# Optimization experiments

Hardware: AMD Instinct MI355X
Metric: run time of the kernel (lower is better)

The kernel has to match this reference:

```python
import jax, jax.numpy as jnp
import numpy as np

B, T, D = 256, 128, 300
H = 512          # lstm_size
NUM_LAYERS = 2
OUT_DIM = 200    # context_encoded_dim
FORGET_BIAS = 1.0


def lstm_layer(x, W, b):
    """BasicLSTMCell over time. x: [B,T,in], W: [in+H,4H], b: [4H] -> [B,T,H].
    Gate order i, j, f, o (TF BasicLSTMCell); c' = c*sig(f+1) + sig(i)*tanh(j)."""
    Bn = x.shape[0]
    c0 = jnp.zeros((Bn, H), x.dtype)
    h0 = jnp.zeros((Bn, H), x.dtype)

    def step(carry, xt):
        c, h = carry
        z = jnp.concatenate([xt, h], axis=-1) @ W + b  # [B,4H]
        i, j, f, o = jnp.split(z, 4, axis=-1)
        c = c * jax.nn.sigmoid(f + FORGET_BIAS) + jax.nn.sigmoid(i) * jnp.tanh(j)
        h = jnp.tanh(c) * jax.nn.sigmoid(o)
        return (c, h), h

    _, hs = jax.lax.scan(step, (c0, h0), jnp.swapaxes(x, 0, 1))  # [T,B,H]
    return jnp.swapaxes(hs, 0, 1)  # [B,T,H]


def encode(x, W0, b0, W1, b1, lengths):
    h = lstm_layer(x, W0, b0)
    h = lstm_layer(h, W1, b1)
    # last valid output per example (dynamic_rnn outputs before `length` are
    # identical to a plain scan; we gather at t = length-1)
    idx = (lengths - 1).astype(jnp.int32)[:, None, None]  # [B,1,1]
    return jnp.take_along_axis(h, idx, axis=1)[:, 0, :]   # [B,H]


def setup_inputs() -> dict:
    key = jax.random.key(0)
    ks = jax.random.split(key, 12)
    s = 1.0 / 100.0

    def gate_w(k, in_dim):
        return jax.random.normal(k, (in_dim + H, 4 * H), jnp.float32) * 0.05

    return {
        "left_embed": jax.random.normal(ks[0], (B, T, D), jnp.float32),
        "right_embed": jax.random.normal(ks[1], (B, T, D), jnp.float32),
        "left_lengths": jax.random.randint(ks[2], (B,), 1, T + 1, jnp.int32),
        "right_lengths": jax.random.randint(ks[3], (B,), 1, T + 1, jnp.int32),
        "lW0": gate_w(ks[4], D),
        "lb0": jnp.zeros((4 * H,), jnp.float32),
        "lW1": gate_w(ks[5], H),
        "lb1": jnp.zeros((4 * H,), jnp.float32),
        "rW0": gate_w(ks[6], D),
        "rb0": jnp.zeros((4 * H,), jnp.float32),
        "rW1": gate_w(ks[7], H),
        "rb1": jnp.zeros((4 * H,), jnp.float32),
        "trans_W": jax.random.normal(ks[8], (2 * H, OUT_DIM), jnp.float32) * s,
    }


def reference(left_embed, right_embed, left_lengths, right_lengths,
              lW0, lb0, lW1, lb1, rW0, rb0, rW1, rb1, trans_W):
    left_last = encode(left_embed, lW0, lb0, lW1, lb1, left_lengths)    # [B,H]
    right_last = encode(right_embed, rW0, rb0, rW1, rb1, right_lengths)  # [B,H]
    ctx = jnp.concatenate([left_last, right_last], axis=1)  # [B,2H]
    return ctx @ trans_W  # [B,OUT_DIM]; dropout keep_prob=1.0 -> identity
```

## Files before the change

### kernel.cpp

```cpp
#include <hip/hip_runtime.h>
#include <hip/hip_bf16.h>
#include <stdint.h>


using short4_t = __attribute__((ext_vector_type(4))) short;
using short8_t = __attribute__((ext_vector_type(8))) short;
using f32x4    = __attribute__((ext_vector_type(4))) float;
using ull2_t   = __attribute__((ext_vector_type(2))) unsigned long long;

#define B_   256
#define T_   128
#define Draw 300
#define Dp   320
#define H_   512
#define G4   2048
#define TC   8
#define MC   (TC * 256)
#define NC   (T_ / TC)
#define FLAG_STRIDE 64

__device__ __forceinline__ short f2bf(float x){
  union { float f; unsigned u; } v; v.f = x;
  unsigned r = (v.u + 0x7FFFu + ((v.u >> 16) & 1u)) >> 16;
  return (short)r;
}
__device__ __forceinline__ float bf2f(short b){
  union { unsigned u; float f; } v; v.u = ((unsigned)(unsigned short)b) << 16;
  return v.f;
}
__device__ __forceinline__ float sigf(float x){ return 1.f / (1.f + __expf(-x)); }
__device__ __forceinline__ float tanh_f(float x){
  x = fmaxf(-15.f, fminf(15.f, x));
  float e = __expf(-2.f * x);
  return (1.f - e) / (1.f + e);
}
__device__ __forceinline__ void gload_lds16(const void* g, void* l){
  __builtin_amdgcn_global_load_lds((const __attribute__((address_space(1))) void*)g,
                                   (__attribute__((address_space(3))) void*)l, 16, 0, 0);
}

__global__ __launch_bounds__(256) void pad_x_chunk(const float* __restrict__ xl,
                                                   const float* __restrict__ xr,
                                                   short* __restrict__ xpadc, int t0)
{
  const int N = 2 * MC * Dp;
  for(int i = blockIdx.x * 256 + threadIdx.x; i < N; i += gridDim.x * 256){
    int side = i / (MC * Dp);
    int rem  = i - side * (MC * Dp);
    int row  = rem / Dp;
    int d    = rem - row * Dp;
    int tl = row >> 8, b = row & 255;
    const float* x = side ? xr : xl;
    float v = (d < Draw) ? x[((size_t)b * T_ + (t0 + tl)) * Draw + d] : 0.f;
    xpadc[i] = f2bf(v);
  }
}

__global__ __launch_bounds__(256) void transpose_w(const float* __restrict__ in,
                                                   short* __restrict__ out,
                                                   int row_off, int krows, int K)
{
  __shared__ float tile[32][33];
  int k0 = blockIdx.x * 32, n0 = blockIdx.y * 32;
  int tx = threadIdx.x & 31, ty = threadIdx.x >> 5;
  #pragma unroll
  for(int p = 0; p < 4; p++){
    int k = k0 + ty + p * 8;
    float v = (k < krows) ? in[(size_t)(k + row_off) * G4 + (n0 + tx)] : 0.f;
    tile[ty + p * 8][tx] = v;
  }
  __syncthreads();
  #pragma unroll
  for(int p = 0; p < 4; p++){
    int n = n0 + ty + p * 8;
    out[(size_t)n * K + k0 + tx] = f2bf(tile[tx][ty + p * 8]);
  }
}

__global__ __launch_bounds__(256, 2) void gemm_zpre(
    const short* __restrict__ Al, const short* __restrict__ Ar,
    const short* __restrict__ Wl, const short* __restrict__ Wr,
    const float* __restrict__ bl, const float* __restrict__ br,
    short* __restrict__ Zl, short* __restrict__ Zr, int K)
{
  __shared__ short As[8192];
  __shared__ short Bs[8192];
  const int side = blockIdx.z;
  const short* A = side ? Ar : Al;
  const short* W = side ? Wr : Wl;
  const float* bias = side ? br : bl;
  short* Zo = side ? Zr : Zl;
  const int m0 = blockIdx.x * 128, n0 = blockIdx.y * 128;
  const int tid = threadIdx.x, l = tid & 63, w = tid >> 6;
  const int wm = w & 1, wn = w >> 1;
  const int ln = l & 15, lq = l >> 4;

  f32x4 acc[4][4];
  const f32x4 z4 = {0.f, 0.f, 0.f, 0.f};
  #pragma unroll
  for(int i = 0; i < 4; i++)
    #pragma unroll
    for(int j = 0; j < 4; j++) acc[i][j] = z4;

  for(int k0 = 0; k0 < K; k0 += 64){
    __syncthreads();
    #pragma unroll
    for(int i = 0; i < 4; i++){
      int qb = w * 256 + i * 64;
      int q  = qb + l;
      int row = q >> 3, c = q & 7, cs = c ^ (row & 7);
      gload_lds16(A + (size_t)(m0 + row) * K + k0 + cs * 8, As + qb * 8);
      gload_lds16(W + (size_t)(n0 + row) * K + k0 + cs * 8, Bs + qb * 8);
    }
    __syncthreads();
    #pragma unroll
    for(int kt = 0; kt < 2; kt++){
      short8_t af[4], bf[4];
      #pragma unroll
      for(int i = 0; i < 4; i++){
        int mr = wm * 64 + i * 16 + ln;
        int nr = wn * 64 + i * 16 + ln;
        int cw = kt * 4 + lq;
        af[i] = *(const short8_t*)(As + (mr * 8 + (cw ^ (mr & 7))) * 8);
        bf[i] = *(const short8_t*)(Bs + (nr * 8 + (cw ^ (nr & 7))) * 8);
      }
      #pragma unroll
      for(int i = 0; i < 4; i++)
        #pragma unroll
        for(int j = 0; j < 4; j++)
          acc[i][j] = __builtin_amdgcn_mfma_f32_16x16x32_bf16(af[i], bf[j], acc[i][j], 0, 0, 0);
    }
  }
  #pragma unroll
  for(int j = 0; j < 4; j++){
    int n = n0 + wn * 64 + j * 16 + ln;
    float bv = bias[n];
    int gn = (n0 >> 4) + wn * 4 + j;
    #pragma unroll
    for(int i = 0; i < 4; i++){
      int gm = (m0 >> 4) + wm * 4 + i;
      short4_t sv;
      #pragma unroll
      for(int r = 0; r < 4; r++) sv[r] = f2bf(acc[i][j][r] + bv);
      *(short4_t*)(Zo + ((size_t)(gm * 128 + gn) * 64 + l) * 4) = sv;
    }
  }
}

__global__ __launch_bounds__(256, 1) void lstm_rec_dual(
    const short* __restrict__ Z0l, const short* __restrict__ Z0r,
    const short* __restrict__ Z1l, const short* __restrict__ Z1r,
    const short* __restrict__ Wt0l, const short* __restrict__ Wt0r,
    const short* __restrict__ Wt1l, const short* __restrict__ Wt1r,
    short* __restrict__ h0l, short* __restrict__ h0r,
    short* __restrict__ h1l, short* __restrict__ h1r,
    float* __restrict__ cstate,
    const int* __restrict__ lenl, const int* __restrict__ lenr,
    float* __restrict__ ctx,
    unsigned* __restrict__ flags, int t0, int has0, int has1)
{
  __shared__ short hlds[32 * 512];
  const int blk = blockIdx.x;
  const int lay  = blk >> 7;
  const int side = (blk >> 6) & 1;
  const int g    = (blk >> 3) & 7;
  const int cb   = blk & 7;
  if(lay ? (!has1) : (!has0)) return;
  const int tid = threadIdx.x, l = tid & 63, w = tid >> 6;
  const int ln = l & 15, lq = l >> 4;
  const short* Z  = lay ? (side ? Z1r : Z1l) : (side ? Z0r : Z0l);
  const short* Wt = lay ? (side ? Wt1r : Wt1l) : (side ? Wt0r : Wt0l);
  short* hseq = lay ? (side ? h1r : h1l) : (side ? h0r : h0l);
  const int mask  = lay ? 1 : (TC - 1);
  const int tbase = lay ? (t0 - TC) : t0;
  const int* len = lay ? (side ? lenr : lenl) : nullptr;
  unsigned* flag = flags + (size_t)((lay * 2 + side) * 8 + g) * FLAG_STRIDE;
  const int hc = cb * 64 + w * 16;
  const int rbase = g * 32;

  short8_t Bf[4][16];
  #pragma unroll
  for(int gate = 0; gate < 4; gate++){
    const short* wp = Wt + (size_t)(gate * 512 + hc + ln) * 512 + lq * 8;
    #pragma unroll
    for(int kt = 0; kt < 16; kt++)
      Bf[gate][kt] = *(const short8_t*)(wp + kt * 32);
  }

  float* cptr = cstate + ((size_t)((lay * 2 + side) * 256 + rbase + lq * 4) * 512) + hc + ln;
  float cst[2][4];
  if(tbase == 0){
    #pragma unroll
    for(int rs = 0; rs < 2; rs++)
      #pragma unroll
      for(int r = 0; r < 4; r++) cst[rs][r] = 0.f;
  } else {
    #pragma unroll
    for(int rs = 0; rs < 2; rs++)
      #pragma unroll
      for(int r = 0; r < 4; r++) cst[rs][r] = cptr[(size_t)(rs * 16 + r) * 512];
  }

  for(int tl = 0; tl < TC; tl++){
    const int t = tbase + tl;
    short4_t zv0[4], zv1[4];
    {
      const int gmb = tl * 16 + g * 2;
      #pragma unroll
      for(int gate = 0; gate < 4; gate++){
        int gn = gate * 32 + cb * 4 + w;
        zv0[gate] = *(const short4_t*)(Z + ((size_t)(gmb * 128 + gn) * 64 + l) * 4);
        zv1[gate] = *(const short4_t*)(Z + ((size_t)((gmb + 1) * 128 + gn) * 64 + l) * 4);
      }
    }
    if(t > 0){
      const unsigned target = 8u * (unsigned)t;
      if(w == 0){
        while(__hip_atomic_load(flag, __ATOMIC_RELAXED, __HIP_MEMORY_SCOPE_AGENT) < target)
          __builtin_amdgcn_s_sleep(2);
      }
      __syncthreads();
      __atomic_signal_fence(__ATOMIC_ACQUIRE);
      const unsigned long long* hsrc = (const unsigned long long*)
          (hseq + ((size_t)(((t - 1) & mask) * 256 + rbase)) * 512);
      #pragma unroll
      for(int it = 0; it < 8; it++){
        int gidx = it * 256 + tid;
        int row = gidx >> 6, s = gidx & 63;
        unsigned long long u0 = __hip_atomic_load(hsrc + (size_t)row * 128 + s * 2,
                                                  __ATOMIC_RELAXED, __HIP_MEMORY_SCOPE_AGENT);
        unsigned long long u1 = __hip_atomic_load(hsrc + (size_t)row * 128 + s * 2 + 1,
                                                  __ATOMIC_RELAXED, __HIP_MEMORY_SCOPE_AGENT);
        int sp = s ^ (row & 7);
        ull2_t uv; uv[0] = u0; uv[1] = u1;
        *(ull2_t*)(hlds + row * 512 + sp * 8) = uv;
      }
      __syncthreads();
    }

#define ROWSET_BODY(RS, ZV)                                                          \
    {                                                                                \
      f32x4 acc[4];                                                                  \
      _Pragma("unroll")                                                              \
      for(int gate = 0; gate < 4; gate++)                                            \
        _Pragma("unroll")                                                            \
        for(int r = 0; r < 4; r++) acc[gate][r] = bf2f(ZV[gate][r]);                 \
      if(t > 0){                                                                     \
        short8_t af[16];                                                             \
        _Pragma("unroll")                                                            \
        for(int kt = 0; kt < 16; kt++){                                              \
          int sp = (kt * 4 + lq) ^ (ln & 7);                                         \
          af[kt] = *(const short8_t*)(hlds + (RS * 16 + ln) * 512 + sp * 8);         \
        }                                                                            \
        _Pragma("unroll")                                                            \
        for(int kt = 0; kt < 16; kt++)                                               \
          _Pragma("unroll")                                                          \
          for(int gate = 0; gate < 4; gate++)                                        \
            acc[gate] = __builtin_amdgcn_mfma_f32_16x16x32_bf16(af[kt], Bf[gate][kt],\
                                                                acc[gate], 0, 0, 0);  \
      }                                                                              \
      float hv[4];                                                                   \
      _Pragma("unroll")                                                              \
      for(int r = 0; r < 4; r++){                                                    \
        float iv = sigf(acc[0][r]);                                                  \
        float jv = tanh_f(acc[1][r]);                                                \
        float fv = sigf(acc[2][r] + 1.0f);                                           \
        float ov = sigf(acc[3][r]);                                                  \
        float c  = cst[RS][r] * fv + iv * jv;                                        \
        cst[RS][r] = c;                                                              \
        hv[r] = tanh_f(c) * ov;                                                      \
      }                                                                              \
      {                                                                              \
        short* hrow = hseq + ((size_t)((t & mask) * 256 + rbase + RS * 16 + lq * 4)) \
                      * 512 + hc + ln;                                               \
        _Pragma("unroll")                                                            \
        for(int r = 0; r < 4; r++){                                                  \
          unsigned lo = (unsigned short)f2bf(hv[r]);                                 \
          unsigned hi = (unsigned short)f2bf(__shfl_xor(hv[r], 1, 64));              \
          unsigned pk = lo | (hi << 16);                                             \
          unsigned pk2 = __shfl_xor(pk, 2, 64);                                      \
          if((ln & 3) == 0){                                                         \
            unsigned long long v = (unsigned long long)pk |                          \
                                   ((unsigned long long)pk2 << 32);                  \
            __hip_atomic_store((unsigned long long*)(hrow + (size_t)r * 512), v,     \
                               __ATOMIC_RELAXED, __HIP_MEMORY_SCOPE_AGENT);          \
          }                                                                          \
        }                                                                            \
      }                                                                              \
      if(len){                                                                       \
        _Pragma("unroll")                                                            \
        for(int r = 0; r < 4; r++){                                                  \
          int b = rbase + RS * 16 + lq * 4 + r;                                      \
          if(len[b] - 1 == t)                                                        \
            ctx[(size_t)b * 1024 + side * 512 + hc + ln] = hv[r];                    \
        }                                                                            \
      }                                                                              \
    }

    ROWSET_BODY(0, zv0)
    ROWSET_BODY(1, zv1)
#undef ROWSET_BODY

    __atomic_signal_fence(__ATOMIC_SEQ_CST);
    asm volatile("s_waitcnt vmcnt(0)" ::: "memory");
    __syncthreads();
    if(tid == 0)
      __hip_atomic_fetch_add(flag, 1u, __ATOMIC_RELEASE, __HIP_MEMORY_SCOPE_AGENT);
  }
  #pragma unroll
  for(int rs = 0; rs < 2; rs++)
    #pragma unroll
    for(int r = 0; r < 4; r++)
      cptr[(size_t)(rs * 16 + r) * 512] = cst[rs][r];
}

__global__ __launch_bounds__(256) void final_mm(const float* __restrict__ ctx,
                                                const float* __restrict__ W,
                                                float* __restrict__ out)
{
  __shared__ float cs[4][1024];
  const int tid = threadIdx.x;
  const int b0 = blockIdx.x * 4;
  for(int i = tid; i < 4 * 1024; i += 256)
    cs[i >> 10][i & 1023] = ctx[(size_t)b0 * 1024 + i];
  __syncthreads();
  if(tid < 200){
    float a0 = 0, a1 = 0, a2 = 0, a3 = 0;
    for(int k = 0; k < 1024; k++){
      float wv = W[k * 200 + tid];
      a0 += cs[0][k] * wv; a1 += cs[1][k] * wv;
      a2 += cs[2][k] * wv; a3 += cs[3][k] * wv;
    }
    out[(size_t)(b0 + 0) * 200 + tid] = a0;
    out[(size_t)(b0 + 1) * 200 + tid] = a1;
    out[(size_t)(b0 + 2) * 200 + tid] = a2;
    out[(size_t)(b0 + 3) * 200 + tid] = a3;
  }
}

extern "C" void kernel_launch(void* const* d_in, const int* in_sizes, int n_in,
                              void* d_out, int out_size, void* d_ws, size_t ws_size,
                              hipStream_t stream)
{
  (void)in_sizes; (void)n_in; (void)out_size; (void)ws_size;
  const float* xl   = (const float*)d_in[0];
  const float* xr   = (const float*)d_in[1];
  const int*   lenl = (const int*)  d_in[2];
  const int*   lenr = (const int*)  d_in[3];
  const float* lW0  = (const float*)d_in[4];
  const float* lb0  = (const float*)d_in[5];
  const float* lW1  = (const float*)d_in[6];
  const float* lb1  = (const float*)d_in[7];
  const float* rW0  = (const float*)d_in[8];
  const float* rb0  = (const float*)d_in[9];
  const float* rW1  = (const float*)d_in[10];
  const float* rb1  = (const float*)d_in[11];
  const float* tW   = (const float*)d_in[12];
  float* out = (float*)d_out;
  char* ws = (char*)d_ws;

  constexpr size_t SZ_WXT0 = (size_t)2048 * Dp * 2;
  constexpr size_t SZ_WT   = (size_t)2048 * 512 * 2;
  constexpr size_t SZ_XPC  = (size_t)2 * MC * Dp * 2;
  constexpr size_t SZ_ZPRE = (size_t)MC * 2048 * 2;
  constexpr size_t SZ_H0   = (size_t)TC * 256 * 512 * 2;
  constexpr size_t SZ_H1   = (size_t)2 * 256 * 512 * 2;
  constexpr size_t SZ_CST  = (size_t)2 * 2 * 256 * 512 * 4;
  constexpr size_t SZ_CTX  = (size_t)256 * 1024 * 4;
  constexpr size_t SZ_FLAGS = (size_t)64 * FLAG_STRIDE * 4;

  size_t off = 0;
  auto carve = [&](size_t sz){ size_t o = off; off += (sz + 255) & ~(size_t)255; return o; };
  size_t o_wxt0_l = carve(SZ_WXT0), o_wxt0_r = carve(SZ_WXT0);
  size_t o_wht0_l = carve(SZ_WT),   o_wht0_r = carve(SZ_WT);
  size_t o_wxt1_l = carve(SZ_WT),   o_wxt1_r = carve(SZ_WT);
  size_t o_wht1_l = carve(SZ_WT),   o_wht1_r = carve(SZ_WT);
  size_t o_xpc    = carve(SZ_XPC);
  size_t o_zp0_l  = carve(SZ_ZPRE), o_zp0_r  = carve(SZ_ZPRE);
  size_t o_zp1_l  = carve(SZ_ZPRE), o_zp1_r  = carve(SZ_ZPRE);
  size_t o_h0_l   = carve(SZ_H0),   o_h0_r   = carve(SZ_H0);
  size_t o_h1_l   = carve(SZ_H1),   o_h1_r   = carve(SZ_H1);
  size_t o_cst    = carve(SZ_CST);
  size_t o_ctx    = carve(SZ_CTX);
  size_t o_flags  = carve(SZ_FLAGS);

  short* wxt0_l = (short*)(ws + o_wxt0_l);
  short* wxt0_r = (short*)(ws + o_wxt0_r);
  short* wht0_l = (short*)(ws + o_wht0_l);
  short* wht0_r = (short*)(ws + o_wht0_r);
  short* wxt1_l = (short*)(ws + o_wxt1_l);
  short* wxt1_r = (short*)(ws + o_wxt1_r);
  short* wht1_l = (short*)(ws + o_wht1_l);
  short* wht1_r = (short*)(ws + o_wht1_r);
  short* xpc_l  = (short*)(ws + o_xpc);
  short* xpc_r  = xpc_l + (size_t)MC * Dp;
  short* zp0_l  = (short*)(ws + o_zp0_l);
  short* zp0_r  = (short*)(ws + o_zp0_r);
  short* zp1_l  = (short*)(ws + o_zp1_l);
  short* zp1_r  = (short*)(ws + o_zp1_r);
  short* h0_l   = (short*)(ws + o_h0_l);
  short* h0_r   = (short*)(ws + o_h0_r);
  short* h1_l   = (short*)(ws + o_h1_l);
  short* h1_r   = (short*)(ws + o_h1_r);
  float* cst    = (float*)(ws + o_cst);
  float* ctx    = (float*)(ws + o_ctx);
  unsigned* flags = (unsigned*)(ws + o_flags);

  hipMemsetAsync(flags, 0, SZ_FLAGS, stream);

  transpose_w<<<dim3(Dp / 32, 64), 256, 0, stream>>>(lW0, wxt0_l,   0, Draw, Dp);
  transpose_w<<<dim3(Dp / 32, 64), 256, 0, stream>>>(rW0, wxt0_r,   0, Draw, Dp);
  transpose_w<<<dim3(16, 64),      256, 0, stream>>>(lW0, wht0_l, 300,  512, 512);
  transpose_w<<<dim3(16, 64),      256, 0, stream>>>(rW0, wht0_r, 300,  512, 512);
  transpose_w<<<dim3(16, 64),      256, 0, stream>>>(lW1, wxt1_l,   0,  512, 512);
  transpose_w<<<dim3(16, 64),      256, 0, stream>>>(rW1, wxt1_r,   0,  512, 512);
  transpose_w<<<dim3(16, 64),      256, 0, stream>>>(lW1, wht1_l, 512,  512, 512);
  transpose_w<<<dim3(16, 64),      256, 0, stream>>>(rW1, wht1_r, 512,  512, 512);

  for(int c = 0; c < NC; c++){
    const int t0 = c * TC;
    pad_x_chunk<<<2048, 256, 0, stream>>>(xl, xr, xpc_l, t0);
    gemm_zpre<<<dim3(MC / 128, 16, 2), 256, 0, stream>>>(xpc_l, xpc_r, wxt0_l, wxt0_r,
                                                         lb0, rb0, zp0_l, zp0_r, Dp);
    if(c > 0)
      gemm_zpre<<<dim3(MC / 128, 16, 2), 256, 0, stream>>>(h0_l, h0_r, wxt1_l, wxt1_r,
                                                           lb1, rb1, zp1_l, zp1_r, 512);
    lstm_rec_dual<<<256, 256, 0, stream>>>(zp0_l, zp0_r, zp1_l, zp1_r,
                                           wht0_l, wht0_r, wht1_l, wht1_r,
                                           h0_l, h0_r, h1_l, h1_r,
                                           cst, lenl, lenr, ctx, flags,
                                           t0, 1, c > 0 ? 1 : 0);
  }
  gemm_zpre<<<dim3(MC / 128, 16, 2), 256, 0, stream>>>(h0_l, h0_r, wxt1_l, wxt1_r,
                                                       lb1, rb1, zp1_l, zp1_r, 512);
  lstm_rec_dual<<<256, 256, 0, stream>>>(zp0_l, zp0_r, zp1_l, zp1_r,
                                         wht0_l, wht0_r, wht1_l, wht1_r,
                                         h0_l, h0_r, h1_l, h1_r,
                                         cst, lenl, lenr, ctx, flags,
                                         NC * TC, 0, 1);

  final_mm<<<64, 256, 0, stream>>>(ctx, tW, out);
}
```

Baseline: 2.457 ms.

## Split per-group step flag into per-column-block flags for finer-grained waiting

Replaces the single counter per (layer, side, row-group), which waited for all 8 column blocks, with one flag per producing column block. Each wave now spin-waits only on the two column blocks whose h slices it copies into LDS and starts loading them as soon as they are ready. The intent is to let blocks begin the next step earlier instead of waiting for the slowest producer. In exchange there are more flags to poll and more atomic traffic, and the flag buffer grows; flag reset and sizing must match the larger layout.

```diff
diff --git a/kernel.cpp b/kernel.cpp
--- a/kernel.cpp
+++ b/kernel.cpp
@@ -18,6 +18,7 @@
 #define MC   (TC * 256)
 #define NC   (T_ / TC)
 #define FLAG_STRIDE 64
+#define NFLAG 256
 
 __device__ __forceinline__ short f2bf(float x){
   union { float f; unsigned u; } v; v.f = x;
@@ -174,7 +175,7 @@
   const int mask  = lay ? 1 : (TC - 1);
   const int tbase = lay ? (t0 - TC) : t0;
   const int* len = lay ? (side ? lenr : lenl) : nullptr;
-  unsigned* flag = flags + (size_t)((lay * 2 + side) * 8 + g) * FLAG_STRIDE;
+  unsigned* flagbase = flags + (size_t)(((lay * 2 + side) * 8 + g) * 8) * FLAG_STRIDE;
   const int hc = cb * 64 + w * 16;
   const int rbase = g * 32;
 
@@ -214,26 +215,31 @@
       }
     }
     if(t > 0){
-      const unsigned target = 8u * (unsigned)t;
-      if(w == 0){
-        while(__hip_atomic_load(flag, __ATOMIC_RELAXED, __HIP_MEMORY_SCOPE_AGENT) < target)
-          __builtin_amdgcn_s_sleep(2);
-      }
-      __syncthreads();
-      __atomic_signal_fence(__ATOMIC_ACQUIRE);
       const unsigned long long* hsrc = (const unsigned long long*)
           (hseq + ((size_t)(((t - 1) & mask) * 256 + rbase)) * 512);
       #pragma unroll
-      for(int it = 0; it < 8; it++){
-        int gidx = it * 256 + tid;
-        int row = gidx >> 6, s = gidx & 63;
-        unsigned long long u0 = __hip_atomic_load(hsrc + (size_t)row * 128 + s * 2,
-                                                  __ATOMIC_RELAXED, __HIP_MEMORY_SCOPE_AGENT);
-        unsigned long long u1 = __hip_atomic_load(hsrc + (size_t)row * 128 + s * 2 + 1,
-                                                  __ATOMIC_RELAXED, __HIP_MEMORY_SCOPE_AGENT);
-        int sp = s ^ (row & 7);
-        ull2_t uv; uv[0] = u0; uv[1] = u1;
-        *(ull2_t*)(hlds + row * 512 + sp * 8) = uv;
+      for(int ss = 0; ss < 2; ss++){
+        const int scb = w * 2 + ss;
+        if(l == 0){
+          const unsigned target = (unsigned)t;
+          while(__hip_atomic_load(flagbase + scb * FLAG_STRIDE, __ATOMIC_RELAXED,
+                                  __HIP_MEMORY_SCOPE_AGENT) < target)
+            __builtin_amdgcn_s_sleep(1);
+        }
+        __atomic_signal_fence(__ATOMIC_ACQUIRE);
+        #pragma unroll
+        for(int it = 0; it < 4; it++){
+          int gidx = it * 64 + l;
+          int row = gidx >> 3, sg = gidx & 7;
+          int gk = scb * 8 + sg;
+          unsigned long long u0 = __hip_atomic_load(hsrc + (size_t)row * 128 + gk * 2,
+                                                    __ATOMIC_RELAXED, __HIP_MEMORY_SCOPE_AGENT);
+          unsigned long long u1 = __hip_atomic_load(hsrc + (size_t)row * 128 + gk * 2 + 1,
+                                                    __ATOMIC_RELAXED, __HIP_MEMORY_SCOPE_AGENT);
+          int sp = gk ^ (row & 7);
+          ull2_t uv; uv[0] = u0; uv[1] = u1;
+          *(ull2_t*)(hlds + row * 512 + sp * 8) = uv;
+        }
       }
       __syncthreads();
     }
@@ -305,7 +311,8 @@
     asm volatile("s_waitcnt vmcnt(0)" ::: "memory");
     __syncthreads();
     if(tid == 0)
-      __hip_atomic_fetch_add(flag, 1u, __ATOMIC_RELEASE, __HIP_MEMORY_SCOPE_AGENT);
+      __hip_atomic_fetch_add(flagbase + cb * FLAG_STRIDE, 1u,
+                             __ATOMIC_RELEASE, __HIP_MEMORY_SCOPE_AGENT);
   }
   #pragma unroll
   for(int rs = 0; rs < 2; rs++)
@@ -367,7 +374,7 @@
   constexpr size_t SZ_H1   = (size_t)2 * 256 * 512 * 2;
   constexpr size_t SZ_CST  = (size_t)2 * 2 * 256 * 512 * 4;
   constexpr size_t SZ_CTX  = (size_t)256 * 1024 * 4;
-  constexpr size_t SZ_FLAGS = (size_t)64 * FLAG_STRIDE * 4;
+  constexpr size_t SZ_FLAGS = (size_t)NFLAG * FLAG_STRIDE * 4;
 
   size_t off = 0;
   auto carve = [&](size_t sz){ size_t o = off; off += (sz + 255) & ~(size_t)255; return o; };
```

Measured after the change: 2.597 ms. 1.06x slower.
